# Kernel optimization log

Measured on AMD Instinct MI355X. Metric: run time of the kernel, lower is better.

Reference implementation:

```python
import jax, jax.numpy as jnp
import numpy as np

EPS = 1e-5
SLOPE = 0.01  # LeakyReLU negative_slope

def _ln(x, g, b):
    m = jnp.mean(x, axis=-1, keepdims=True)
    v = jnp.mean((x - m) ** 2, axis=-1, keepdims=True)
    return (x - m) * jax.lax.rsqrt(v + EPS) * g + b

def _lrelu(x):
    return jnp.where(x >= 0, x, SLOPE * x)

def _s6(x, W1, b1, W2, b2, W3, b3, A):
    # x: (B, L, D); A: (D, N). Mamba-style S6 selective scan.
    Bm = x @ W2 + b2                       # (B, L, N) input-dependent B
    Cm = x @ W3 + b3                       # (B, L, N) input-dependent C
    delta = jax.nn.softplus(x @ W1 + b1)   # (B, L, D) step sizes
    dA = jnp.exp(jnp.einsum('bld,dn->bldn', delta, A))            # (B,L,D,N)
    dBx = jnp.einsum('bld,bln->bldn', delta, Bm) * x[..., None]    # (B,L,D,N) dB * x
    Bsz, L, D = x.shape
    N = A.shape[1]
    def step(h, inp):
        dA_t, dBx_t, C_t = inp
        h = dA_t * h + dBx_t                       # (B, D, N)
        return h, jnp.einsum('bn,bdn->bd', C_t, h)  # y_t: (B, D)
    xs = (jnp.transpose(dA, (1, 0, 2, 3)),
          jnp.transpose(dBx, (1, 0, 2, 3)),
          jnp.transpose(Cm, (1, 0, 2)))
    _, ys = jax.lax.scan(step, jnp.zeros((Bsz, D, N), x.dtype), xs)
    return jnp.transpose(ys, (1, 0, 2))  # (B, L, D)

def _fwd(text, audio, video, tW1, tb1, tg1, tbe1, tW2, tb2, tg2, tbe2, sW1, sb1, sW2, sb2, sW3, sb3, sA, aW1, ab1, ag1, abe1, aW2, ab2, ag2, abe2, vW1, vb1, vg1, vbe1, vW2, vb2, vg2, vbe2, cW1, cb1, cW2, cb2):
    # text branch: Linear+LN+LeakyReLU x2, Dropout(eval=identity), S6
    t = _lrelu(_ln(text @ tW1 + tb1, tg1, tbe1))
    t = _lrelu(_ln(t @ tW2 + tb2, tg2, tbe2))
    t = _s6(t, sW1, sb1, sW2, sb2, sW3, sb3, sA)
    # audio / video branches are computed but do not feed the output (as in source)
    a = _lrelu(_ln(audio @ aW1 + ab1, ag1, abe1))
    a = _lrelu(_ln(a @ aW2 + ab2, ag2, abe2))
    v = _lrelu(_ln(video @ vW1 + vb1, vg1, vbe1))
    v = _lrelu(_ln(v @ vW2 + vb2, vg2, vbe2))
    o1 = t @ cW1 + cb1
    return o1 @ cW2 + cb2  # (B, L, 2)

def setup_inputs() -> dict:
    key = jax.random.key(0)
    ks = iter(jax.random.split(key, 64))
    def W(shape, s=0.05):
        return jax.random.normal(next(ks), shape, jnp.float32) * s
    B, L = 64, 63
    d = {
        'text': jax.random.normal(next(ks), (B, L, 100), jnp.float32),
        'audio': jax.random.normal(next(ks), (B, L, 73), jnp.float32),
        'video': jax.random.normal(next(ks), (B, L, 100), jnp.float32),
        'tW1': W((100, 128)), 'tb1': jnp.zeros(128), 'tg1': jnp.ones(128), 'tbe1': jnp.zeros(128),
        'tW2': W((128, 100)), 'tb2': jnp.zeros(100), 'tg2': jnp.ones(100), 'tbe2': jnp.zeros(100),
        'sW1': W((100, 100)), 'sb1': jnp.zeros(100),
        'sW2': W((100, 300)), 'sb2': jnp.zeros(300),
        'sW3': W((100, 300)), 'sb3': jnp.zeros(300),
        'sA': jnp.full((100, 300), 1.0 / np.sqrt(300.0), jnp.float32),  # F.normalize(ones, dim=-1)
        'aW1': W((73, 256)), 'ab1': jnp.zeros(256), 'ag1': jnp.ones(256), 'abe1': jnp.zeros(256),
        'aW2': W((256, 100)), 'ab2': jnp.zeros(100), 'ag2': jnp.ones(100), 'abe2': jnp.zeros(100),
        'vW1': W((100, 256)), 'vb1': jnp.zeros(256), 'vg1': jnp.ones(256), 'vbe1': jnp.zeros(256),
        'vW2': W((256, 100)), 'vb2': jnp.zeros(100), 'vg2': jnp.ones(100), 'vbe2': jnp.zeros(100),
        'cW1': W((100, 50)), 'cb1': jnp.zeros(50),
        'cW2': W((50, 2)), 'cb2': jnp.zeros(2),
    }
    return d

def reference(text, audio, video, tW1, tb1, tg1, tbe1, tW2, tb2, tg2, tbe2, sW1, sb1, sW2, sb2, sW3, sb3, sA, aW1, ab1, ag1, abe1, aW2, ab2, ag2, abe2, vW1, vb1, vg1, vbe1, vW2, vb2, vg2, vbe2, cW1, cb1, cW2, cb2):
    return _fwd(text, audio, video, tW1, tb1, tg1, tbe1, tW2, tb2, tg2, tbe2, sW1, sb1, sW2, sb2, sW3, sb3, sA, aW1, ab1, ag1, abe1, aW2, ab2, ag2, abe2, vW1, vb1, vg1, vbe1, vW2, vb2, vg2, vbe2, cW1, cb1, cW2, cb2)
```

## Files before the change

### kernel.cpp

```cpp
#include <hip/hip_runtime.h>
#include <hip/hip_bf16.h>


typedef __hip_bfloat16 bf16;

#define BATCH 64
#define SEQ   63
#define ROWS  (BATCH * SEQ)
#define DIN   100
#define H1    128
#define DM    100
#define NS    300

__device__ __forceinline__ float2 up2(unsigned u) {
    float2 r;
    r.x = __uint_as_float(u << 16);
    r.y = __uint_as_float(u & 0xffff0000u);
    return r;
}
template<bool ISB>
__device__ __forceinline__ float LD(const void* p, int i) {
    if (ISB) return __bfloat162float(((const bf16*)p)[i]);
    else     return ((const float*)p)[i];
}
template<bool ISB>
__device__ __forceinline__ float2 LD2(const void* p, int i) {
    if (ISB) return up2(((const unsigned*)p)[i]);
    else     return ((const float2*)p)[i];
}
__device__ __forceinline__ float waveReduceSum(float v) {
#pragma unroll
    for (int off = 32; off > 0; off >>= 1) v += __shfl_xor(v, off, 64);
    return v;
}
__device__ __forceinline__ float4 waveReduceSum4(float4 v) {
#pragma unroll
    for (int off = 32; off > 0; off >>= 1) {
        const float a = __shfl_xor(v.x, off, 64);
        const float b = __shfl_xor(v.y, off, 64);
        const float c = __shfl_xor(v.z, off, 64);
        const float d = __shfl_xor(v.w, off, 64);
        v.x += a; v.y += b; v.z += c; v.w += d;
    }
    return v;
}
__device__ __forceinline__ float lrelu(float x) { return x >= 0.f ? x : 0.01f * x; }
__device__ __forceinline__ float softplusf(float x) {
    return (x > 20.f) ? x : log1pf(__expf(x));
}
__device__ __forceinline__ bool flags_uniform(const float* __restrict__ f) {
    bool u = true;
#pragma unroll
    for (int i = 0; i < 8; ++i) u &= (f[i] > 0.5f);
    return u;
}
__device__ __forceinline__ bool detect_bf16(const unsigned short* __restrict__ probe) {
    const int l = threadIdx.x & 63;
    const unsigned u0 = probe[l * 2];
    const unsigned u1 = probe[l * 2 + 1];
    const float v0 = fabsf(__uint_as_float(u0 << 16));
    const float v1 = fabsf(__uint_as_float(u1 << 16));
    const bool big = !(v0 < 1000.f) || !(v1 < 1000.f);
    const bool zero_even = (u0 == 0u);
    const unsigned long long mb = __ballot(big);
    const unsigned long long mz = __ballot(zero_even);
    return (mb == 0ULL) && (__popcll(mz) < 32);
}

template<bool ISB>
__device__ __forceinline__ void a_main(
    const void* __restrict__ text,
    const void* __restrict__ tW1, const void* __restrict__ tb1,
    const void* __restrict__ tg1, const void* __restrict__ tbe1,
    const void* __restrict__ tW2, const void* __restrict__ tb2,
    const void* __restrict__ tg2, const void* __restrict__ tbe2,
    const void* __restrict__ sW1w, const void* __restrict__ sb1,
    float* __restrict__ ddx, float* __restrict__ t2g,
    float* __restrict__ sW,
    float (&xb)[4][DIN][2], float (&t1b)[4][H1][2], float (&t2b)[4][DM][2])
{
    const int tid  = threadIdx.x;
    const int w    = tid >> 6;
    const int lane = tid & 63;
    const int r0   = blockIdx.x * 8 + w * 2;

    if (lane < 50) {
#pragma unroll
        for (int r = 0; r < 2; ++r) {
            const float2 xv = LD2<ISB>(text, (r0 + r) * 50 + lane);
            xb[w][2 * lane][r]     = xv.x;
            xb[w][2 * lane + 1][r] = xv.y;
        }
    }
    for (int i = tid; i < 6400; i += 256)
        *(float2*)&sW[2 * i] = LD2<ISB>(tW1, i);
    __syncthreads();

    const float2 b1v = LD2<ISB>(tb1, lane);
    float ax0 = b1v.x, ay0 = b1v.y, ax1 = b1v.x, ay1 = b1v.y;
#pragma unroll 10
    for (int k = 0; k < DIN; ++k) {
        const float2 wv = *(const float2*)&sW[k * 128 + 2 * lane];
        const float2 xv = *(const float2*)&xb[w][k][0];
        ax0 += xv.x * wv.x; ay0 += xv.x * wv.y;
        ax1 += xv.y * wv.x; ay1 += xv.y * wv.y;
    }
    {
        float4 red = waveReduceSum4(make_float4(
            ax0 + ay0, ax0 * ax0 + ay0 * ay0,
            ax1 + ay1, ax1 * ax1 + ay1 * ay1));
        const float m0 = red.x * (1.f / 128.f);
        const float rs0 = rsqrtf(red.y * (1.f / 128.f) - m0 * m0 + 1e-5f);
        const float m1 = red.z * (1.f / 128.f);
        const float rs1 = rsqrtf(red.w * (1.f / 128.f) - m1 * m1 + 1e-5f);
        const float2 g = LD2<ISB>(tg1, lane), be = LD2<ISB>(tbe1, lane);
        float2 v;
        v.x = lrelu((ax0 - m0) * rs0 * g.x + be.x);
        v.y = lrelu((ax1 - m1) * rs1 * g.x + be.x);
        *(float2*)&t1b[w][2 * lane][0] = v;
        v.x = lrelu((ay0 - m0) * rs0 * g.y + be.y);
        v.y = lrelu((ay1 - m1) * rs1 * g.y + be.y);
        *(float2*)&t1b[w][2 * lane + 1][0] = v;
    }
    __syncthreads();

    for (int i = tid; i < 6400; i += 256)
        *(float2*)&sW[2 * i] = LD2<ISB>(tW2, i);
    __syncthreads();

    const bool act = lane < 50;
    const int  li  = act ? lane : 0;
    const float2 b2v = LD2<ISB>(tb2, li);
    float cx0 = b2v.x, cy0 = b2v.y, cx1 = b2v.x, cy1 = b2v.y;
#pragma unroll 8
    for (int k = 0; k < H1; ++k) {
        const float2 wv = *(const float2*)&sW[k * 100 + 2 * li];
        const float2 tv = *(const float2*)&t1b[w][k][0];
        cx0 += tv.x * wv.x; cy0 += tv.x * wv.y;
        cx1 += tv.y * wv.x; cy1 += tv.y * wv.y;
    }
    float u0x, u0y, u1x, u1y;
    {
        float4 red = waveReduceSum4(act ? make_float4(
            cx0 + cy0, cx0 * cx0 + cy0 * cy0,
            cx1 + cy1, cx1 * cx1 + cy1 * cy1) : make_float4(0.f, 0.f, 0.f, 0.f));
        const float m0 = red.x * 0.01f;
        const float rs0 = rsqrtf(red.y * 0.01f - m0 * m0 + 1e-5f);
        const float m1 = red.z * 0.01f;
        const float rs1 = rsqrtf(red.w * 0.01f - m1 * m1 + 1e-5f);
        if (act) {
            const float2 g = LD2<ISB>(tg2, lane), be = LD2<ISB>(tbe2, lane);
            u0x = lrelu((cx0 - m0) * rs0 * g.x + be.x);
            u0y = lrelu((cy0 - m0) * rs0 * g.y + be.y);
            u1x = lrelu((cx1 - m1) * rs1 * g.x + be.x);
            u1y = lrelu((cy1 - m1) * rs1 * g.y + be.y);
            t2b[w][2 * lane][0] = u0x; t2b[w][2 * lane + 1][0] = u0y;
            t2b[w][2 * lane][1] = u1x; t2b[w][2 * lane + 1][1] = u1y;
            *(float2*)(t2g + (r0)     * DM + 2 * lane) = make_float2(u0x, u0y);
            *(float2*)(t2g + (r0 + 1) * DM + 2 * lane) = make_float2(u1x, u1y);
        }
    }
    __syncthreads();

    for (int i = tid; i < 5000; i += 256)
        *(float2*)&sW[2 * i] = LD2<ISB>(sW1w, i);
    __syncthreads();

    const float2 sbv = LD2<ISB>(sb1, li);
    float dA0x = sbv.x, dA0y = sbv.y, dA1x = sbv.x, dA1y = sbv.y;
#pragma unroll 10
    for (int k = 0; k < DM; ++k) {
        const float2 wv = *(const float2*)&sW[k * 100 + 2 * li];
        const float2 tv = *(const float2*)&t2b[w][k][0];
        dA0x += tv.x * wv.x; dA0y += tv.x * wv.y;
        dA1x += tv.y * wv.x; dA1y += tv.y * wv.y;
    }
    if (act) {
        float de0 = softplusf(dA0x), de1 = softplusf(dA0y);
        float4 o;
        o.x = de0; o.y = de0 * u0x; o.z = de1; o.w = de1 * u0y;
        *(float4*)(ddx + (r0) * (2 * DM) + 4 * lane) = o;
        de0 = softplusf(dA1x); de1 = softplusf(dA1y);
        o.x = de0; o.y = de0 * u1x; o.z = de1; o.w = de1 * u1y;
        *(float4*)(ddx + (r0 + 1) * (2 * DM) + 4 * lane) = o;
    }
}

template<bool ISB>
__device__ __forceinline__ void a_prep(
    const void* __restrict__ sW2, const void* __restrict__ sb2,
    const void* __restrict__ sW3, const void* __restrict__ sb3,
    float* __restrict__ M33p, float* __restrict__ k0w, float* __restrict__ sW,
    int d3)
{
    const int tid = threadIdx.x;
    const int w = tid >> 6, lane = tid & 63;
    float* W3row = sW;
    float* b2v   = sW + 320;
    float* b3v   = sW + 640;
    for (int i = tid; i < 300; i += 256) {
        W3row[i] = LD<ISB>(sW3, d3 * 300 + i);
        b2v[i]   = LD<ISB>(sb2, i);
        b3v[i]   = LD<ISB>(sb3, i);
    }
    __syncthreads();
    for (int g = 0; g < 6; ++g) {
        const int d2 = w * 25 + g * 4;
        float4 p = make_float4(0.f, 0.f, 0.f, 0.f);
#pragma unroll
        for (int rep = 0; rep < 5; ++rep) {
            const int n = lane + 64 * rep;
            if (n < 300) {
                const float w3 = W3row[n];
                p.x += LD<ISB>(sW2, (d2 + 0) * 300 + n) * w3;
                p.y += LD<ISB>(sW2, (d2 + 1) * 300 + n) * w3;
                p.z += LD<ISB>(sW2, (d2 + 2) * 300 + n) * w3;
                p.w += LD<ISB>(sW2, (d2 + 3) * 300 + n) * w3;
            }
        }
        p = waveReduceSum4(p);
        if (lane == 0) {
            M33p[d3 * 102 + d2 + 0] = p.x;
            M33p[d3 * 102 + d2 + 1] = p.y;
            M33p[d3 * 102 + d2 + 2] = p.z;
            M33p[d3 * 102 + d2 + 3] = p.w;
        }
    }
    {
        const int d2 = w * 25 + 24;
        float4 p = make_float4(0.f, 0.f, 0.f, 0.f);
#pragma unroll
        for (int rep = 0; rep < 5; ++rep) {
            const int n = lane + 64 * rep;
            if (n < 300) {
                p.x += LD<ISB>(sW2, d2 * 300 + n) * W3row[n];
                if (w == 0) p.y += W3row[n] * b2v[n];
                if (w == 1) p.y += LD<ISB>(sW2, d3 * 300 + n) * b3v[n];
                if (w == 2 && d3 == 0) p.y += b2v[n] * b3v[n];
            }
        }
        p = waveReduceSum4(p);
        if (lane == 0) {
            M33p[d3 * 102 + d2] = p.x;
            if (w == 0) M33p[d3 * 102 + 100] = p.y;
            if (w == 1) M33p[d3 * 102 + 101] = p.y;
            if (w == 2 && d3 == 0) k0w[0] = p.y;
        }
    }
}

template<bool ISB>
__device__ __forceinline__ void a_check(
    const void* __restrict__ sA, float* __restrict__ Afl,
    float* __restrict__ sW, int j)
{
    const int tid = threadIdx.x;
    const float a0 = LD<ISB>(sA, 0);
    bool ok = true;
    for (int i = j * 3750 + tid; i < (j + 1) * 3750; i += 256)
        ok &= (LD<ISB>(sA, i) == a0);
    if (tid == 0) sW[960] = 1.f;
    __syncthreads();
    if (!ok) sW[960] = 0.f;
    __syncthreads();
    if (tid == 0) Afl[j] = sW[960];
    if (j == 0 && tid == 1) Afl[8] = a0;
}

template<bool ISB>
__device__ __forceinline__ void a_mkv(
    const void* __restrict__ cW1, const void* __restrict__ cb1,
    const void* __restrict__ cW2, const void* __restrict__ cb2,
    float* __restrict__ Mkv)
{
    const int t = threadIdx.x;
    if (t < 200) {
        const int d = t >> 1, j = t & 1;
        float m = 0.f;
#pragma unroll 5
        for (int i = 0; i < 50; ++i)
            m += LD<ISB>(cW1, d * 50 + i) * LD<ISB>(cW2, 2 * i + j);
        Mkv[t] = m;
    } else if (t < 202) {
        const int j = t - 200;
        float kv = LD<ISB>(cb2, j);
#pragma unroll 5
        for (int i = 0; i < 50; ++i)
            kv += LD<ISB>(cb1, i) * LD<ISB>(cW2, 2 * i + j);
        Mkv[200 + j] = kv;
    }
}

__global__ __launch_bounds__(256) void k_A(
    const void* text,
    const void* tW1, const void* tb1, const void* tg1, const void* tbe1,
    const void* tW2, const void* tb2, const void* tg2, const void* tbe2,
    const void* sW1w, const void* sb1,
    const void* sW2, const void* sb2, const void* sW3, const void* sb3,
    const void* sA,
    const void* cW1, const void* cb1, const void* cW2, const void* cb2,
    float* ddx, float* t2g, float* Mkv, float* M33p, float* k0w, float* Afl,
    const unsigned short* probe)
{
    __shared__ __align__(16) float sW[12800];
    __shared__ __align__(16) float xb[4][DIN][2];
    __shared__ __align__(16) float t1b[4][H1][2];
    __shared__ __align__(16) float t2b[4][DM][2];
    const bool isb = detect_bf16(probe);
    const int blk = blockIdx.x;
    if (blk < 504) {
        if (isb) a_main<true >(text, tW1, tb1, tg1, tbe1, tW2, tb2, tg2, tbe2,
                               sW1w, sb1, ddx, t2g, sW, xb, t1b, t2b);
        else     a_main<false>(text, tW1, tb1, tg1, tbe1, tW2, tb2, tg2, tbe2,
                               sW1w, sb1, ddx, t2g, sW, xb, t1b, t2b);
    } else if (blk < 604) {
        if (isb) a_prep<true >(sW2, sb2, sW3, sb3, M33p, k0w, sW, blk - 504);
        else     a_prep<false>(sW2, sb2, sW3, sb3, M33p, k0w, sW, blk - 504);
    } else if (blk < 612) {
        if (isb) a_check<true >(sA, Afl, sW, blk - 604);
        else     a_check<false>(sA, Afl, sW, blk - 604);
    } else {
        if (isb) a_mkv<true >(cW1, cb1, cW2, cb2, Mkv);
        else     a_mkv<false>(cW1, cb1, cW2, cb2, Mkv);
    }
}

__global__ __launch_bounds__(256) void k_G(
    const float* __restrict__ t2g, const float* __restrict__ M33p,
    const float* __restrict__ k0w, float* __restrict__ G,
    const float* __restrict__ Afl)
{
    __shared__ __align__(16) float sT2[64 * 102];
    __shared__ __align__(16) float sZ[8][104];
    __shared__ float srv[64];
    __shared__ float sv[100];
    if (!flags_uniform(Afl)) return;
    const int b  = blockIdx.x >> 3;
    const int tc = blockIdx.x & 7;
    const int tid = threadIdx.x;
    const int w = tid >> 6, lane = tid & 63;

    for (int i = tid; i < 3150; i += 256) {
        const float2 v = *(const float2*)(t2g + b * 6300 + 2 * i);
        const int t = i / 50, k = 2 * (i % 50);
        sT2[t * 102 + k]     = v.x;
        sT2[t * 102 + k + 1] = v.y;
    }
    if (tid < 100) sv[tid] = M33p[tid * 102 + 101];
    __syncthreads();

    if (lane < 16) {
        const int s = w * 16 + lane;
        if (s < SEQ) {
            float acc = 0.f;
#pragma unroll 4
            for (int k = 0; k < 100; ++k) acc += sT2[s * 102 + k] * sv[k];
            srv[s] = acc;
        }
    }

    {
        const int l2 = (lane < 51) ? 2 * lane : 0;
        int tg2i[2];
#pragma unroll
        for (int r = 0; r < 2; ++r) {
            const int t = tc * 8 + w * 2 + r;
            tg2i[r] = (t < SEQ) ? t : SEQ - 1;
        }
        float2 acc[2];
        acc[0] = make_float2(0.f, 0.f);
        acc[1] = make_float2(0.f, 0.f);
        float2 ring[10];
#pragma unroll
        for (int j = 0; j < 10; ++j) ring[j] = *(const float2*)(M33p + j * 102 + l2);
        for (int kk = 0; kk < 100; kk += 10) {
#pragma unroll
            for (int j = 0; j < 10; ++j) {
                const int jj = kk + j;
                const float2 wv = ring[j];
                if (jj + 10 < 100) ring[j] = *(const float2*)(M33p + (jj + 10) * 102 + l2);
#pragma unroll
                for (int r = 0; r < 2; ++r) {
                    const float tv = sT2[tg2i[r] * 102 + jj];
                    acc[r].x += tv * wv.x;
                    acc[r].y += tv * wv.y;
                }
            }
        }
        if (lane < 51) {
#pragma unroll
            for (int r = 0; r < 2; ++r)
                *(float2*)&sZ[w * 2 + r][l2] = acc[r];
        }
    }
    __syncthreads();

    const float kz = k0w[0];
    const int s = lane;
    const int sc = (s < SEQ) ? s : SEQ - 1;
#pragma unroll
    for (int r = 0; r < 2; ++r) {
        const int tl = w * 2 + r;
        const int t  = tc * 8 + tl;
        float acc = kz + sZ[tl][100] + srv[sc];
#pragma unroll 5
        for (int k2 = 0; k2 < 50; ++k2) {
            const float2 z  = *(const float2*)&sZ[tl][2 * k2];
            const float2 tv = *(const float2*)&sT2[sc * 102 + 2 * k2];
            acc += z.x * tv.x + z.y * tv.y;
        }
        if (t < SEQ && s < SEQ) G[b * 3969 + t * 63 + s] = acc;
    }
}

__global__ __launch_bounds__(256) void k_Y(
    const float* __restrict__ ddx, const float* __restrict__ G,
    float* __restrict__ yT, const float* __restrict__ Afl)
{
    __shared__ __align__(16) float sG[63][64];
    __shared__ __align__(16) float sDD[63][28];
    __shared__ __align__(16) float sV[13][68];
    __shared__ float sE[63][16];
    if (!flags_uniform(Afl)) return;
    const float a = Afl[8];
    const int b = blockIdx.x >> 3, c = blockIdx.x & 7;
    const int dbase = 13 * c;
    const int tid = threadIdx.x;

    for (int i = tid; i < 3969; i += 256) {
        const int t = i / 63, s = i - t * 63;
        sG[t][s] = G[b * 3969 + i];
    }
    for (int i = tid; i < 819; i += 256) {
        const int t = i / 13, dd = i - t * 13;
        if (dbase + dd < DM) {
            const float2 v = *(const float2*)(ddx + (b * SEQ + t) * 200 + 2 * (dbase + dd));
            sDD[t][2 * dd]     = v.x;
            sDD[t][2 * dd + 1] = v.y;
        }
    }
    __syncthreads();
    if (tid < 13 && dbase + tid < DM) {
        float D = 0.f;
        for (int t = 0; t < SEQ; ++t) {
            D += sDD[t][2 * tid];
            const float E = __expf(a * D);
            sE[t][tid] = E;
            sV[tid][t] = sDD[t][2 * tid + 1] / E;
        }
    }
    __syncthreads();
    for (int o = tid; o < 819; o += 256) {
        const int t = o / 13, dd = o - t * 13;
        if (dbase + dd >= DM) continue;
        const int lim = t + 1, q = lim & ~3;
        float acc = 0.f;
        int s = 0;
        for (; s < q; s += 4) {
            const float4 g = *(const float4*)&sG[t][s];
            const float4 v = *(const float4*)&sV[dd][s];
            acc += g.x * v.x + g.y * v.y + g.z * v.z + g.w * v.w;
        }
        for (; s < lim; ++s) acc += sG[t][s] * sV[dd][s];
        yT[(dbase + dd) * ROWS + b * SEQ + t] = sE[t][dd] * acc;
    }
}

template<bool ISB>
__device__ __forceinline__ float4 LD4(const void* p, int i) {
    if (ISB) {
        const uint2 u = ((const uint2*)p)[i];
        float4 r;
        r.x = __uint_as_float(u.x << 16);
        r.y = __uint_as_float(u.x & 0xffff0000u);
        r.z = __uint_as_float(u.y << 16);
        r.w = __uint_as_float(u.y & 0xffff0000u);
        return r;
    } else return ((const float4*)p)[i];
}

template<bool ISB>
__device__ __forceinline__ void b_impl(
    const float* __restrict__ t2g,
    const void* __restrict__ sW2, const void* __restrict__ sb2,
    const void* __restrict__ sW3, const void* __restrict__ sb3,
    float* __restrict__ BC, float (&sT)[DM][8])
{
    const int t  = threadIdx.x;
    const int r0 = blockIdx.x * 8;
    if (t < DM) {
#pragma unroll
        for (int r = 0; r < 8; ++r) sT[t][r] = t2g[(r0 + r) * DM + t];
    }
    __syncthreads();
    const bool isB = t < 75;
    const bool valid = t < 150;
    const int colbase = isB ? 4 * t : (valid ? 4 * (t - 75) : 0);
    const void* Wp   = isB ? sW2 : sW3;
    const void* bias = isB ? sb2 : sb3;
    const int rs4 = NS >> 2;
    const int cb4 = colbase >> 2;
    float4 acc[8];
    {
        const float4 bv = LD4<ISB>(bias, cb4);
#pragma unroll
        for (int r = 0; r < 8; ++r) acc[r] = bv;
    }
    float4 ring[4];
#pragma unroll
    for (int j = 0; j < 4; ++j) ring[j] = LD4<ISB>(Wp, j * rs4 + cb4);
    for (int kk = 0; kk < DM; kk += 4) {
#pragma unroll
        for (int j = 0; j < 4; ++j) {
            const int k = kk + j;
            const float4 wv = ring[j];
            if (k + 4 < DM) ring[j] = LD4<ISB>(Wp, (k + 4) * rs4 + cb4);
            const float4 lo = *(const float4*)&sT[k][0];
            const float4 hi = *(const float4*)&sT[k][4];
            acc[0].x += lo.x * wv.x; acc[0].y += lo.x * wv.y; acc[0].z += lo.x * wv.z; acc[0].w += lo.x * wv.w;
            acc[1].x += lo.y * wv.x; acc[1].y += lo.y * wv.y; acc[1].z += lo.y * wv.z; acc[1].w += lo.y * wv.w;
            acc[2].x += lo.z * wv.x; acc[2].y += lo.z * wv.y; acc[2].z += lo.z * wv.z; acc[2].w += lo.z * wv.w;
            acc[3].x += lo.w * wv.x; acc[3].y += lo.w * wv.y; acc[3].z += lo.w * wv.z; acc[3].w += lo.w * wv.w;
            acc[4].x += hi.x * wv.x; acc[4].y += hi.x * wv.y; acc[4].z += hi.x * wv.z; acc[4].w += hi.x * wv.w;
            acc[5].x += hi.y * wv.x; acc[5].y += hi.y * wv.y; acc[5].z += hi.y * wv.z; acc[5].w += hi.y * wv.w;
            acc[6].x += hi.z * wv.x; acc[6].y += hi.z * wv.y; acc[6].z += hi.z * wv.z; acc[6].w += hi.z * wv.w;
            acc[7].x += hi.w * wv.x; acc[7].y += hi.w * wv.y; acc[7].z += hi.w * wv.z; acc[7].w += hi.w * wv.w;
        }
    }
    if (valid) {
        const int off = isB ? 0 : 1;
#pragma unroll
        for (int r = 0; r < 8; ++r) {
            float* bp = BC + (r0 + r) * (2 * NS) + 2 * colbase + off;
            bp[0] = acc[r].x; bp[2] = acc[r].y;
            bp[4] = acc[r].z; bp[6] = acc[r].w;
        }
    }
}

__global__ __launch_bounds__(192, 1) void k_B(
    const float* t2g, const void* sW2, const void* sb2,
    const void* sW3, const void* sb3, float* BC,
    const float* Afl, const unsigned short* probe)
{
    __shared__ __align__(16) float sT[DM][8];
    if (flags_uniform(Afl)) return;
    if (detect_bf16(probe)) b_impl<true >(t2g, sW2, sb2, sW3, sb3, BC, sT);
    else                    b_impl<false>(t2g, sW2, sb2, sW3, sb3, BC, sT);
}

template<bool ISB>
__device__ __forceinline__ void scan_impl(
    const float* __restrict__ ddx, const float* __restrict__ BC,
    const void* __restrict__ sA, float* __restrict__ y,
    float (&sacc)[4][16][2][68])
{
    const int w    = threadIdx.x >> 6;
    const int lane = threadIdx.x & 63;
    const int wid  = blockIdx.x * 4 + w;
    const int b    = wid / 50;
    const int dp   = wid % 50;
    const int d0   = 2 * dp, d1 = d0 + 1;

    int nc[5]; bool nv[5];
    float A0[5], A1[5], h0[5], h1[5];
#pragma unroll
    for (int c = 0; c < 5; ++c) {
        const int n = lane + 64 * c;
        nv[c] = n < NS;
        nc[c] = nv[c] ? n : 0;
        A0[c] = nv[c] ? LD<ISB>(sA, d0 * NS + nc[c]) : 0.f;
        A1[c] = nv[c] ? LD<ISB>(sA, d1 * NS + nc[c]) : 0.f;
        h0[c] = 0.f; h1[c] = 0.f;
    }
    const float* ddp = ddx + (b * SEQ) * (2 * DM) + 4 * dp;
    const float* BCp = BC  + (b * SEQ) * (2 * NS);
    float*       yp  = y   + (b * SEQ) * DM + d0;

    float4 pdd[3];
    float2 pbc[3][5];
#pragma unroll
    for (int j = 0; j < 3; ++j) {
        pdd[j] = *(const float4*)(ddp + j * (2 * DM));
#pragma unroll
        for (int c = 0; c < 5; ++c)
            pbc[j][c] = nv[c] ? *(const float2*)(BCp + j * (2 * NS) + 2 * nc[c])
                              : make_float2(0.f, 0.f);
    }
    const int pr = lane >> 1;
    const int hh = lane & 1;
    const int sa = pr & 15;
    const int aa = pr >> 4;

#pragma unroll 3
    for (int l = 0; l < SEQ; ++l) {
        const int bi = l % 3;
        const float4 dd = pdd[bi];
        float2 bc[5];
#pragma unroll
        for (int c = 0; c < 5; ++c) bc[c] = pbc[bi][c];
        if (l + 3 < SEQ) {
            pdd[bi] = *(const float4*)(ddp + (l + 3) * (2 * DM));
#pragma unroll
            for (int c = 0; c < 5; ++c)
                pbc[bi][c] = nv[c] ? *(const float2*)(BCp + (l + 3) * (2 * NS) + 2 * nc[c])
                                   : make_float2(0.f, 0.f);
        }
        float a0 = 0.f, a1 = 0.f;
#pragma unroll
        for (int c = 0; c < 5; ++c) {
            h0[c] = __expf(dd.x * A0[c]) * h0[c] + dd.y * bc[c].x;
            a0 += bc[c].y * h0[c];
            h1[c] = __expf(dd.z * A1[c]) * h1[c] + dd.w * bc[c].x;
            a1 += bc[c].y * h1[c];
        }
        const int s = l & 15;
        sacc[w][s][0][lane] = a0;
        sacc[w][s][1][lane] = a1;

        if (s == 15 || l == SEQ - 1) {
            const int l0 = l & ~15;
            const int cs = l - l0 + 1;
            float sum = 0.f;
            if (sa < cs) {
                const float* rowp = &sacc[w][sa][aa][hh * 32];
#pragma unroll
                for (int i = 0; i < 8; ++i) {
                    const float4 v = *(const float4*)(rowp + 4 * i);
                    sum += v.x + v.y + v.z + v.w;
                }
            }
            sum += __shfl_xor(sum, 1, 64);
            if (hh == 0 && sa < cs) yp[(l0 + sa) * DM + aa] = sum;
        }
    }
}

__global__ __launch_bounds__(256) void k_scan(
    const float* ddx, const float* BC, const void* sA, float* y,
    const float* Afl, const unsigned short* probe)
{
    __shared__ __align__(16) float sacc[4][16][2][68];
    if (flags_uniform(Afl)) return;
    if (detect_bf16(probe)) scan_impl<true >(ddx, BC, sA, y, sacc);
    else                    scan_impl<false>(ddx, BC, sA, y, sacc);
}

template<bool ISB>
__device__ __forceinline__ void head_impl(
    const float* __restrict__ y, const float* __restrict__ Mkv,
    void* __restrict__ outp, bool fast)
{
    const int row = blockIdx.x * 256 + threadIdx.x;
    if (row >= ROWS) return;
    float a0 = Mkv[200], a1 = Mkv[201];
    if (fast) {
#pragma unroll 4
        for (int k = 0; k < DM; ++k) {
            const float v = y[k * ROWS + row];
            const float2 m = *(const float2*)(Mkv + 2 * k);
            a0 += v * m.x;
            a1 += v * m.y;
        }
    } else {
        const float* yr = y + row * DM;
#pragma unroll 4
        for (int k = 0; k < DM; ++k) {
            const float v = yr[k];
            const float2 m = *(const float2*)(Mkv + 2 * k);
            a0 += v * m.x;
            a1 += v * m.y;
        }
    }
    if (ISB) {
        ((bf16*)outp)[row * 2 + 0] = __float2bfloat16(a0);
        ((bf16*)outp)[row * 2 + 1] = __float2bfloat16(a1);
    } else {
        *(float2*)((float*)outp + row * 2) = make_float2(a0, a1);
    }
}

__global__ __launch_bounds__(256) void k_head(
    const float* y, const float* Mkv, void* outp,
    const float* Afl, const unsigned short* probe)
{
    const bool fast = flags_uniform(Afl);
    if (detect_bf16(probe)) head_impl<true >(y, Mkv, outp, fast);
    else                    head_impl<false>(y, Mkv, outp, fast);
}

extern "C" void kernel_launch(void* const* d_in, const int* in_sizes, int n_in,
                              void* d_out, int out_size, void* d_ws, size_t ws_size,
                              hipStream_t stream)
{
    const void* text = d_in[0];
    const void* tW1  = d_in[3];
    const void* tb1  = d_in[4];
    const void* tg1  = d_in[5];
    const void* tbe1 = d_in[6];
    const void* tW2  = d_in[7];
    const void* tb2  = d_in[8];
    const void* tg2  = d_in[9];
    const void* tbe2 = d_in[10];
    const void* sW1  = d_in[11];
    const void* sb1  = d_in[12];
    const void* sW2  = d_in[13];
    const void* sb2  = d_in[14];
    const void* sW3  = d_in[15];
    const void* sb3  = d_in[16];
    const void* sA   = d_in[17];
    const void* cW1  = d_in[34];
    const void* cb1  = d_in[35];
    const void* cW2  = d_in[36];
    const void* cb2  = d_in[37];
    const unsigned short* probe = (const unsigned short*)d_in[3];

    float* ws   = (float*)d_ws;
    float* ddx  = ws;
    float* BCv  = ddx + ROWS * 2 * DM;
    float* Gv   = BCv;
    float* yv   = BCv + ROWS * 2 * NS;
    float* Mkv  = yv + ROWS * DM;
    float* M33p = Mkv + 202;
    float* k0w  = M33p + 10200;
    float* Afl  = k0w + 1;
    float* t2g  = yv;

    k_A<<<613, 256, 0, stream>>>(
        text, tW1, tb1, tg1, tbe1, tW2, tb2, tg2, tbe2,
        sW1, sb1, sW2, sb2, sW3, sb3, sA,
        cW1, cb1, cW2, cb2,
        ddx, t2g, Mkv, M33p, k0w, Afl, probe);

    k_B<<<ROWS / 8, 192, 0, stream>>>(t2g, sW2, sb2, sW3, sb3, BCv, Afl, probe);

    k_G<<<BATCH * 8, 256, 0, stream>>>(t2g, M33p, k0w, Gv, Afl);

    k_Y<<<BATCH * 8, 256, 0, stream>>>(ddx, Gv, yv, Afl);

    k_scan<<<3200 / 4, 256, 0, stream>>>(ddx, BCv, sA, yv, Afl, probe);

    k_head<<<(ROWS + 255) / 256, 256, 0, stream>>>(yv, Mkv, d_out, Afl, probe);
}
```

Measured before the change: 193.1 us.

## Fuse G, Y and head kernels into one per-batch-tile kernel on the fast path

Merges the G-matrix computation, the causal Y contraction and the output head into a single kernel, so G and y no longer go through global memory and two launches disappear on the uniform-A path. Each block now recomputes the cumulative exp scan for all 100 channels over its time prefix and reduces the head projection with a wave reduction. This duplicates scan work across the 8 time tiles of each batch and uses more shared memory per block, which may lower occupancy. The slow-path head kernel now returns early when flags are uniform.

```diff
diff --git a/kernel.cpp b/kernel.cpp
--- a/kernel.cpp
+++ b/kernel.cpp
@@ -325,16 +325,16 @@
     }
 }
 
-__global__ __launch_bounds__(256) void k_G(
-    const float* __restrict__ t2g, const float* __restrict__ M33p,
-    const float* __restrict__ k0w, float* __restrict__ G,
-    const float* __restrict__ Afl)
-{
-    __shared__ __align__(16) float sT2[64 * 102];
-    __shared__ __align__(16) float sZ[8][104];
-    __shared__ float srv[64];
-    __shared__ float sv[100];
-    if (!flags_uniform(Afl)) return;
+template<bool ISB>
+__device__ __forceinline__ void gyh_impl(
+    const float* __restrict__ t2g, const float* __restrict__ ddx,
+    const float* __restrict__ M33p, const float* __restrict__ k0w,
+    const float* __restrict__ Mkv, const float* __restrict__ Afl,
+    void* __restrict__ outp,
+    float* __restrict__ sT2, float (&sZ)[8][104],
+    float* __restrict__ sv, float* __restrict__ srv,
+    float (&sG)[8][64], float* __restrict__ sV, float (&sE)[8][100])
+{
     const int b  = blockIdx.x >> 3;
     const int tc = blockIdx.x & 7;
     const int tid = threadIdx.x;
@@ -395,75 +395,107 @@
     }
     __syncthreads();
 
-    const float kz = k0w[0];
-    const int s = lane;
-    const int sc = (s < SEQ) ? s : SEQ - 1;
-#pragma unroll
-    for (int r = 0; r < 2; ++r) {
-        const int tl = w * 2 + r;
-        const int t  = tc * 8 + tl;
-        float acc = kz + sZ[tl][100] + srv[sc];
+    {
+        const float kz = k0w[0];
+        const int s = lane;
+        const int sc = (s < SEQ) ? s : SEQ - 1;
+        float acc0 = kz + sZ[w * 2][100]     + srv[sc];
+        float acc1 = kz + sZ[w * 2 + 1][100] + srv[sc];
 #pragma unroll 5
         for (int k2 = 0; k2 < 50; ++k2) {
-            const float2 z  = *(const float2*)&sZ[tl][2 * k2];
             const float2 tv = *(const float2*)&sT2[sc * 102 + 2 * k2];
-            acc += z.x * tv.x + z.y * tv.y;
-        }
-        if (t < SEQ && s < SEQ) G[b * 3969 + t * 63 + s] = acc;
-    }
-}
-
-__global__ __launch_bounds__(256) void k_Y(
-    const float* __restrict__ ddx, const float* __restrict__ G,
-    float* __restrict__ yT, const float* __restrict__ Afl)
-{
-    __shared__ __align__(16) float sG[63][64];
-    __shared__ __align__(16) float sDD[63][28];
-    __shared__ __align__(16) float sV[13][68];
-    __shared__ float sE[63][16];
+            const float2 z0 = *(const float2*)&sZ[w * 2][2 * k2];
+            const float2 z1 = *(const float2*)&sZ[w * 2 + 1][2 * k2];
+            acc0 += z0.x * tv.x + z0.y * tv.y;
+            acc1 += z1.x * tv.x + z1.y * tv.y;
+        }
+        if (s < SEQ) {
+            if (tc * 8 + w * 2     < SEQ) sG[w * 2][s]     = acc0;
+            if (tc * 8 + w * 2 + 1 < SEQ) sG[w * 2 + 1][s] = acc1;
+        }
+    }
+    __syncthreads();
+
+    {
+        const float a = Afl[8];
+        const int tmax = (tc * 8 + 7 < SEQ) ? tc * 8 + 7 : SEQ - 1;
+        if (tid < 100) {
+            const int d = tid;
+            float D = 0.f;
+            for (int s = 0; s <= tmax; ++s) {
+                const float2 dn = *(const float2*)(ddx + (b * SEQ + s) * 200 + 2 * d);
+                D += dn.x;
+                const float E = __expf(a * D);
+                sV[d * 65 + s] = dn.y / E;
+                const int tl = s - tc * 8;
+                if (tl >= 0) sE[tl][d] = E;
+            }
+        }
+    }
+    __syncthreads();
+
+    {
+        const int li = (lane < 50) ? lane : 49;
+        const float4 mk = *(const float4*)(Mkv + 4 * li);
+        float4 oacc = make_float4(0.f, 0.f, 0.f, 0.f);
+#pragma unroll
+        for (int r = 0; r < 2; ++r) {
+            const int tl = w * 2 + r;
+            const int t  = tc * 8 + tl;
+            if (t >= SEQ) continue;
+            float acc0 = 0.f, acc1 = 0.f;
+            const float* v0 = sV + (2 * li) * 65;
+            const float* v1 = sV + (2 * li + 1) * 65;
+            for (int s = 0; s <= t; ++s) {
+                const float g = sG[tl][s];
+                acc0 += g * v0[s];
+                acc1 += g * v1[s];
+            }
+            const float2 E = *(const float2*)&sE[tl][2 * li];
+            const float y0 = (lane < 50) ? E.x * acc0 : 0.f;
+            const float y1 = (lane < 50) ? E.y * acc1 : 0.f;
+            if (r == 0) { oacc.x = y0 * mk.x + y1 * mk.z; oacc.y = y0 * mk.y + y1 * mk.w; }
+            else        { oacc.z = y0 * mk.x + y1 * mk.z; oacc.w = y0 * mk.y + y1 * mk.w; }
+        }
+        oacc = waveReduceSum4(oacc);
+        if (lane == 0) {
+            const float kv0 = Mkv[200], kv1 = Mkv[201];
+#pragma unroll
+            for (int r = 0; r < 2; ++r) {
+                const int t = tc * 8 + w * 2 + r;
+                if (t >= SEQ) continue;
+                const int row = b * SEQ + t;
+                const float o0 = (r == 0 ? oacc.x : oacc.z) + kv0;
+                const float o1 = (r == 0 ? oacc.y : oacc.w) + kv1;
+                if (ISB) {
+                    ((bf16*)outp)[row * 2 + 0] = __float2bfloat16(o0);
+                    ((bf16*)outp)[row * 2 + 1] = __float2bfloat16(o1);
+                } else {
+                    *(float2*)((float*)outp + row * 2) = make_float2(o0, o1);
+                }
+            }
+        }
+    }
+}
+
+__global__ __launch_bounds__(256) void k_GYH(
+    const float* __restrict__ t2g, const float* __restrict__ ddx,
+    const float* __restrict__ M33p, const float* __restrict__ k0w,
+    const float* __restrict__ Mkv, const float* __restrict__ Afl,
+    void* __restrict__ outp, const unsigned short* __restrict__ probe)
+{
+    __shared__ __align__(16) float sT2[64 * 102];
+    __shared__ __align__(16) float sZ[8][104];
+    __shared__ float sv[100];
+    __shared__ float srv[64];
+    __shared__ __align__(16) float sG[8][64];
+    __shared__ __align__(16) float sV[100 * 65];
+    __shared__ __align__(16) float sE[8][100];
     if (!flags_uniform(Afl)) return;
-    const float a = Afl[8];
-    const int b = blockIdx.x >> 3, c = blockIdx.x & 7;
-    const int dbase = 13 * c;
-    const int tid = threadIdx.x;
-
-    for (int i = tid; i < 3969; i += 256) {
-        const int t = i / 63, s = i - t * 63;
-        sG[t][s] = G[b * 3969 + i];
-    }
-    for (int i = tid; i < 819; i += 256) {
-        const int t = i / 13, dd = i - t * 13;
-        if (dbase + dd < DM) {
-            const float2 v = *(const float2*)(ddx + (b * SEQ + t) * 200 + 2 * (dbase + dd));
-            sDD[t][2 * dd]     = v.x;
-            sDD[t][2 * dd + 1] = v.y;
-        }
-    }
-    __syncthreads();
-    if (tid < 13 && dbase + tid < DM) {
-        float D = 0.f;
-        for (int t = 0; t < SEQ; ++t) {
-            D += sDD[t][2 * tid];
-            const float E = __expf(a * D);
-            sE[t][tid] = E;
-            sV[tid][t] = sDD[t][2 * tid + 1] / E;
-        }
-    }
-    __syncthreads();
-    for (int o = tid; o < 819; o += 256) {
-        const int t = o / 13, dd = o - t * 13;
-        if (dbase + dd >= DM) continue;
-        const int lim = t + 1, q = lim & ~3;
-        float acc = 0.f;
-        int s = 0;
-        for (; s < q; s += 4) {
-            const float4 g = *(const float4*)&sG[t][s];
-            const float4 v = *(const float4*)&sV[dd][s];
-            acc += g.x * v.x + g.y * v.y + g.z * v.z + g.w * v.w;
-        }
-        for (; s < lim; ++s) acc += sG[t][s] * sV[dd][s];
-        yT[(dbase + dd) * ROWS + b * SEQ + t] = sE[t][dd] * acc;
-    }
+    if (detect_bf16(probe))
+        gyh_impl<true >(t2g, ddx, M33p, k0w, Mkv, Afl, outp, sT2, sZ, sv, srv, sG, sV, sE);
+    else
+        gyh_impl<false>(t2g, ddx, M33p, k0w, Mkv, Afl, outp, sT2, sZ, sv, srv, sG, sV, sE);
 }
 
 template<bool ISB>
@@ -647,30 +679,20 @@
 }
 
 template<bool ISB>
-__device__ __forceinline__ void head_impl(
+__device__ __forceinline__ void headf_impl(
     const float* __restrict__ y, const float* __restrict__ Mkv,
-    void* __restrict__ outp, bool fast)
+    void* __restrict__ outp)
 {
     const int row = blockIdx.x * 256 + threadIdx.x;
     if (row >= ROWS) return;
     float a0 = Mkv[200], a1 = Mkv[201];
-    if (fast) {
+    const float* yr = y + row * DM;
 #pragma unroll 4
-        for (int k = 0; k < DM; ++k) {
-            const float v = y[k * ROWS + row];
-            const float2 m = *(const float2*)(Mkv + 2 * k);
-            a0 += v * m.x;
-            a1 += v * m.y;
-        }
-    } else {
-        const float* yr = y + row * DM;
-#pragma unroll 4
-        for (int k = 0; k < DM; ++k) {
-            const float v = yr[k];
-            const float2 m = *(const float2*)(Mkv + 2 * k);
-            a0 += v * m.x;
-            a1 += v * m.y;
-        }
+    for (int k = 0; k < DM; ++k) {
+        const float v = yr[k];
+        const float2 m = *(const float2*)(Mkv + 2 * k);
+        a0 += v * m.x;
+        a1 += v * m.y;
     }
     if (ISB) {
         ((bf16*)outp)[row * 2 + 0] = __float2bfloat16(a0);
@@ -680,13 +702,13 @@
     }
 }
 
-__global__ __launch_bounds__(256) void k_head(
+__global__ __launch_bounds__(256) void k_headF(
     const float* y, const float* Mkv, void* outp,
     const float* Afl, const unsigned short* probe)
 {
-    const bool fast = flags_uniform(Afl);
-    if (detect_bf16(probe)) head_impl<true >(y, Mkv, outp, fast);
-    else                    head_impl<false>(y, Mkv, outp, fast);
+    if (flags_uniform(Afl)) return;
+    if (detect_bf16(probe)) headf_impl<true >(y, Mkv, outp);
+    else                    headf_impl<false>(y, Mkv, outp);
 }
 
 extern "C" void kernel_launch(void* const* d_in, const int* in_sizes, int n_in,
@@ -718,7 +740,6 @@
     float* ws   = (float*)d_ws;
     float* ddx  = ws;
     float* BCv  = ddx + ROWS * 2 * DM;
-    float* Gv   = BCv;
     float* yv   = BCv + ROWS * 2 * NS;
     float* Mkv  = yv + ROWS * DM;
     float* M33p = Mkv + 202;
@@ -732,13 +753,10 @@
         cW1, cb1, cW2, cb2,
         ddx, t2g, Mkv, M33p, k0w, Afl, probe);
 
+    k_GYH<<<BATCH * 8, 256, 0, stream>>>(t2g, ddx, M33p, k0w, Mkv, Afl,
+                                         d_out, probe);
+
     k_B<<<ROWS / 8, 192, 0, stream>>>(t2g, sW2, sb2, sW3, sb3, BCv, Afl, probe);
-
-    k_G<<<BATCH * 8, 256, 0, stream>>>(t2g, M33p, k0w, Gv, Afl);
-
-    k_Y<<<BATCH * 8, 256, 0, stream>>>(ddx, Gv, yv, Afl);
-
     k_scan<<<3200 / 4, 256, 0, stream>>>(ddx, BCv, sA, yv, Afl, probe);
-
-    k_head<<<(ROWS + 255) / 256, 256, 0, stream>>>(yv, Mkv, d_out, Afl, probe);
-}
+    k_headF<<<(ROWS + 255) / 256, 256, 0, stream>>>(yv, Mkv, d_out, Afl, probe);
+}
```

After: 223.5 us. +15.8%, slower.
